# Kernel optimization log

Measured on AMD Instinct MI355X. Metric: run time of the kernel, lower is better.

## Reference

```python
import jax, jax.numpy as jnp
import numpy as np

NUM_NODES = 512
INPUT_DIM = 64
HID_DIM = 64
K_DIFF = 2          # max_diffusion_step
N_LAYERS = 2
N_SUPPORTS = 1      # filter_type='laplacian'
NUM_MATS = N_SUPPORTS * K_DIFF + 1
CONCAT = INPUT_DIM + HID_DIM  # == HID_DIM + HID_DIM since input_dim == hid_dim


def setup_inputs() -> dict:
    key = jax.random.key(0)
    ks = jax.random.split(key, 8)
    T, B = 48, 32
    inputs = jax.random.normal(ks[0], (T, B, NUM_NODES * INPUT_DIM), dtype=jnp.float32)
    h0 = jnp.zeros((N_LAYERS, B, NUM_NODES * HID_DIM), dtype=jnp.float32)
    supports = jax.random.uniform(ks[1], (N_SUPPORTS, NUM_NODES, NUM_NODES), dtype=jnp.float32) / NUM_NODES
    s = 0.05
    W_gate = jax.random.normal(ks[2], (N_LAYERS, NUM_MATS * CONCAT, 2 * HID_DIM), dtype=jnp.float32) * s
    b_gate = jnp.ones((N_LAYERS, 2 * HID_DIM), dtype=jnp.float32)  # bias_start=1.0
    W_c = jax.random.normal(ks[3], (N_LAYERS, NUM_MATS * CONCAT, HID_DIM), dtype=jnp.float32) * s
    b_c = jnp.zeros((N_LAYERS, HID_DIM), dtype=jnp.float32)
    return {"inputs": inputs, "initial_hidden_state": h0, "supports": supports,
            "W_gate": W_gate, "b_gate": b_gate, "W_c": W_c, "b_c": b_c}


def _gconv(supports, x_flat, h_flat, W, b, out_dim):
    # x_flat: (B, N*d_in), h_flat: (B, N*hid)
    B = x_flat.shape[0]
    xh = jnp.concatenate([x_flat.reshape(B, NUM_NODES, -1),
                          h_flat.reshape(B, NUM_NODES, -1)], axis=-1)  # (B,N,c)
    mats = [xh]
    for i in range(N_SUPPORTS):
        S = supports[i]
        t0, t1 = xh, jnp.einsum('nm,bmc->bnc', S, xh)
        mats.append(t1)
        for _ in range(2, K_DIFF + 1):  # Chebyshev recurrence: x_k = 2 S x_{k-1} - x_{k-2}
            t2 = 2.0 * jnp.einsum('nm,bmc->bnc', S, t1) - t0
            mats.append(t2)
            t0, t1 = t1, t2
    feat = jnp.concatenate(mats, axis=-1)            # (B, N, NUM_MATS*c)
    out = jnp.einsum('bnf,fo->bno', feat, W) + b      # (B, N, out_dim)
    return out


def _dcgru_cell(supports, x, h, Wg, bg, Wc, bc):
    B = x.shape[0]
    gates = jax.nn.sigmoid(_gconv(supports, x, h, Wg, bg, 2 * HID_DIM))  # (B,N,2h)
    r, u = jnp.split(gates, 2, axis=-1)
    rh = (r * h.reshape(B, NUM_NODES, HID_DIM)).reshape(B, NUM_NODES * HID_DIM)
    c = jnp.tanh(_gconv(supports, x, rh, Wc, bc, HID_DIM))               # (B,N,h)
    h3 = h.reshape(B, NUM_NODES, HID_DIM)
    new_h = u * h3 + (1.0 - u) * c
    return new_h.reshape(B, NUM_NODES * HID_DIM)


def reference(inputs, initial_hidden_state, supports, W_gate, b_gate, W_c, b_c):
    current = inputs  # (T, B, N*d)
    final_hidden = []
    for l in range(N_LAYERS):
        def step(h, x, l=l):
            h2 = _dcgru_cell(supports, x, h, W_gate[l], b_gate[l], W_c[l], b_c[l])
            return h2, h2
        hT, outs = jax.lax.scan(step, initial_hidden_state[l], current)
        final_hidden.append(hT)
        current = outs
    return jnp.stack(final_hidden, axis=0), current
```

## Files before the change

kernel.cpp:

```cpp
#include <hip/hip_runtime.h>
#include <math.h>

typedef __bf16 bf16_t;
typedef bf16_t bf16x8 __attribute__((ext_vector_type(8)));
typedef bf16_t bf16x4 __attribute__((ext_vector_type(4)));
typedef float  f32x4  __attribute__((ext_vector_type(4)));
typedef unsigned long long u64_t;

#define NB 32
#define NN 512
#define NH 64
#define NF 384
#define TSTEPS 48

static __device__ __forceinline__ f32x4 mfma16(bf16x8 a, bf16x8 b, f32x4 c){
  return __builtin_amdgcn_mfma_f32_16x16x32_bf16(a, b, c, 0, 0, 0);
}
static __device__ __forceinline__ void gload16(char* lds, const char* g){
  __builtin_amdgcn_global_load_lds((const __attribute__((address_space(1))) void*)g,
                                   (__attribute__((address_space(3))) void*)lds, 16, 0, 0);
}
static __device__ __forceinline__ unsigned pack2(float a, float b){
  bf16_t x = (bf16_t)a, y = (bf16_t)b;
  unsigned short ux = __builtin_bit_cast(unsigned short, x);
  unsigned short uy = __builtin_bit_cast(unsigned short, y);
  return (unsigned)ux | ((unsigned)uy << 16);
}

__global__ __launch_bounds__(256) void k_s2f(const float* __restrict__ S,
                                             float* __restrict__ S2f){
  int idx = blockIdx.x * 256 + threadIdx.x;
  int n = idx >> 9, m = idx & 511;
  float acc = 0.f;
  #pragma unroll 8
  for (int k = 0; k < 512; ++k) acc += S[n * 512 + k] * S[k * 512 + m];
  S2f[idx] = acc;
}

__global__ __launch_bounds__(256) void k_prepS(const float* __restrict__ S,
                                               const float* __restrict__ S2f,
                                               char* __restrict__ dst){
  int id = blockIdx.x * 256 + threadIdx.x;
  int r = id >> 9, k = id & 511;
  float v = (r < 512) ? S[r * 512 + k] : S2f[(r - 512) * 512 + k];
  int rt = r >> 5, rr = r & 31, kt = k >> 6, kk = k & 63;
  size_t off = ((size_t)(rt * 8 + kt)) * 4096 + (size_t)(((rr * 128 + 2 * kk)) ^ ((rr & 7) << 4));
  *(bf16_t*)(dst + off) = (bf16_t)v;
}

__global__ __launch_bounds__(256) void k_prepW(const float* __restrict__ W,
                                               char* __restrict__ dst, int OD){
  int i = blockIdx.x * 256 + threadIdx.x;
  int total = 2 * NF * OD;
  if (i >= total) return;
  int l = i / (NF * OD), rem = i - l * (NF * OD);
  int o = rem / NF, f = rem - o * NF;
  const float* Wl = W + (size_t)l * NF * OD;
  float v;
  if (f < 128)      v = Wl[f * OD + o] - Wl[(256 + f) * OD + o];
  else if (f < 256) v = Wl[f * OD + o];
  else              v = 2.f * Wl[f * OD + o];
  int kt = f >> 6, kk = f & 63;
  size_t off = (size_t)l * (6 * OD * 128) + (size_t)kt * (OD * 128)
             + (size_t)(((o * 128 + 2 * kk)) ^ ((o & 7) << 4));
  *(bf16_t*)(dst + off) = (bf16_t)v;
}

__global__ __launch_bounds__(256) void k_hinit(const float* __restrict__ h0,
                                               float* __restrict__ hNf,
                                               bf16_t* __restrict__ hN){
  size_t i = ((size_t)blockIdx.x * 256 + threadIdx.x) * 8;
  f32x4 a = *(const f32x4*)&h0[i], b = *(const f32x4*)&h0[i + 4];
  *(f32x4*)&hNf[i] = a; *(f32x4*)&hNf[i + 4] = b;
  bf16x8 v;
  #pragma unroll
  for (int q = 0; q < 4; ++q){ v[q] = (bf16_t)a[q]; v[q + 4] = (bf16_t)b[q]; }
  *(bf16x8*)&hN[i] = v;
}

__global__ __launch_bounds__(512, 4) void k_gate(
    const float* __restrict__ inputs, const float* __restrict__ curp, int p,
    const bf16_t* __restrict__ hN, const char* __restrict__ SP,
    const char* __restrict__ WgP, const float* __restrict__ bga,
    bf16_t* __restrict__ rhN, float* __restrict__ uN, bf16_t* __restrict__ Dx)
{
  const int l = blockIdx.y;
  const int t = p - l;
  if (t < 0 || t >= TSTEPS) return;

  __shared__ char smem[81920];
  char* const A0 = smem;            char* const A1 = smem + 16384;
  char* const B0 = smem + 32768;    char* const B1 = smem + 49152;
  char* const FT = smem;
  char* const W0 = smem + 49152;    char* const W1 = smem + 65536;
  char* const RL = smem + 49152;
  char* const UL = smem + 57344;

  const int L = blockIdx.x;
  const int b  = (L & 7) + ((L >> 6) << 3);
  const int bx = (L >> 3) & 7;
  const int n0 = bx * 64;
  const int tid = threadIdx.x, lane = tid & 63, w = tid >> 6;
  const int fr = lane & 15, ko = (lane >> 4) * 8, ro = (lane >> 4) * 4;
  const int pp = tid >> 4, q4 = tid & 15;
  const int wr = w >> 2, wc = w & 3;
  const int wn = w & 1, wo = w >> 1;

  const float* xall = l ? curp : inputs;
  const float*  xs = xall + ((size_t)t * NB + b) * NN * NH;
  const bf16_t* hbg = hN + ((size_t)(l * NB + b)) * NN * NH;
  const char* const WgPl = WgP + (size_t)l * 98304;
  const float* const bg = bga + l * 128;
  bf16_t* const rh_l = rhN + (size_t)l * NB * NN * NH;
  float*  const u_l  = uN  + (size_t)l * NB * NN * NH;
  bf16_t* const Dx_l = Dx  + (size_t)l * NB * NN * 128;

  f32x4 acc[4][2] = {};
  f32x4 rx0[2], rx1[2]; u64_t rh0[2], rh1[2];
  char* const Abuf[2] = { A0, A1 };
  char* const Bbuf[2] = { B0, B1 };

  auto ldB = [&](int kt, int s){
    int m = kt * 64 + 2 * pp;
    const float* xr = xs + (size_t)m * NH + q4 * 4;
    rx0[s] = *(const f32x4*)xr; rx1[s] = *(const f32x4*)(xr + NH);
    const bf16_t* hr = hbg + (size_t)m * NH + q4 * 4;
    rh0[s] = *(const u64_t*)hr; rh1[s] = *(const u64_t*)(hr + NH);
  };
  auto stB = [&](int s, char* Bb){
    int mby = 4 * pp;
    #pragma unroll
    for (int i = 0; i < 4; ++i){
      int c = q4 * 4 + i;
      *(unsigned*)(Bb + ((c * 128 + mby) ^ (((c >> 2) & 7) << 4))) = pack2(rx0[s][i], rx1[s][i]);
      int c2 = c + 64;
      unsigned uh = (unsigned)((rh0[s] >> (16 * i)) & 0xffffULL)
                  | ((unsigned)((rh1[s] >> (16 * i)) & 0xffffULL) << 16);
      *(unsigned*)(Bb + ((c2 * 128 + mby) ^ (((c2 >> 2) & 7) << 4))) = uh;
    }
  };
  auto gloadA = [&](int kt, char* Ab){
    #pragma unroll
    for (int i = 0; i < 2; ++i){
      int c = w * 2 + i;
      int ti = c >> 2;
      int rt = (ti < 2) ? (bx * 2 + ti) : (16 + bx * 2 + (ti - 2));
      gload16(Ab + c * 1024,
              SP + ((size_t)(rt * 8 + kt)) * 4096 + (c & 3) * 1024 + lane * 16);
    }
  };
  auto dmm = [&](const char* Ab, const char* Bb){
    #pragma unroll
    for (int kh = 0; kh < 2; ++kh){
      int kb = 2 * (kh * 32 + ko);
      bf16x8 af[4], bf_[2];
      #pragma unroll
      for (int fm = 0; fm < 4; ++fm){
        int r = wr * 64 + fm * 16 + fr;
        af[fm] = *(const bf16x8*)(Ab + (r >> 5) * 4096 + ((((r & 31) * 128 + kb)) ^ ((r & 7) << 4)));
      }
      #pragma unroll
      for (int fc = 0; fc < 2; ++fc){
        int c = wc * 32 + fc * 16 + fr;
        bf_[fc] = *(const bf16x8*)(Bb + ((c * 128 + kb) ^ (((c >> 2) & 7) << 4)));
      }
      #pragma unroll
      for (int fm = 0; fm < 4; ++fm)
        #pragma unroll
        for (int fc = 0; fc < 2; ++fc)
          acc[fm][fc] = mfma16(af[fm], bf_[fc], acc[fm][fc]);
    }
  };

  ldB(0, 0); stB(0, B0);
  ldB(1, 1);
  gloadA(0, A0);
  __syncthreads();

  #pragma unroll
  for (int kt = 0; kt < 8; ++kt){
    if (kt < 7){
      stB((kt + 1) & 1, Bbuf[(kt + 1) & 1]);
      gloadA(kt + 1, Abuf[(kt + 1) & 1]);
    }
    dmm(Abuf[kt & 1], Bbuf[kt & 1]);
    __syncthreads();
    if (kt < 6) ldB(kt + 2, (kt + 2) & 1);
  }

  #pragma unroll
  for (int s = 0; s < 2; ++s){
    int i = tid + s * 512;
    int row = i >> 4, c8 = (i & 15) * 8;
    char* fdst = FT + (((row * 768 + 2 * c8)) ^ ((row & 7) << 4));
    if (c8 < 64){
      const float* xr = xs + (size_t)(n0 + row) * NH + c8;
      f32x4 a = *(const f32x4*)xr, bq = *(const f32x4*)(xr + 4);
      bf16x8 v;
      #pragma unroll
      for (int q = 0; q < 4; ++q){ v[q] = (bf16_t)a[q]; v[q + 4] = (bf16_t)bq[q]; }
      *(bf16x8*)fdst = v;
    } else {
      *(bf16x8*)fdst = *(const bf16x8*)(hbg + (size_t)(n0 + row) * NH + (c8 - 64));
    }
  }
  #pragma unroll
  for (int fm = 0; fm < 4; ++fm)
    #pragma unroll
    for (int fc = 0; fc < 2; ++fc)
      #pragma unroll
      for (int q = 0; q < 4; ++q){
        int dr = wr * 64 + fm * 16 + ro + q;
        int nn = dr & 63;
        int col = ((dr < 64) ? 128 : 256) + wc * 32 + fc * 16 + fr;
        *(bf16_t*)(FT + (((nn * 768 + 2 * col)) ^ ((nn & 7) << 4))) = (bf16_t)acc[fm][fc][q];
      }

  auto gloadW = [&](int j, char* Wb){
    const char* src = WgPl + (size_t)j * 16384 + (w * 64 + lane) * 16;
    gload16(Wb + w * 1024, src);
    gload16(Wb + 8192 + w * 1024, src + 8192);
  };
  gloadW(0, W0);
  __syncthreads();

  #pragma unroll
  for (int s = 0; s < 2; ++s){
    int i = tid + s * 512;
    int row = i >> 4, d8 = (i & 15) * 8;
    int col = (d8 < 64) ? 128 + d8 : 256 + (d8 - 64);
    bf16x8 v = *(const bf16x8*)(FT + (((row * 768 + 2 * col)) ^ ((row & 7) << 4)));
    *(bf16x8*)&Dx_l[((size_t)b * NN + n0 + row) * 128 + d8] = v;
  }

  f32x4 gd[2][2] = {};
  #pragma unroll
  for (int j = 0; j < 6; ++j){
    if (j < 5) gloadW(j + 1, ((j + 1) & 1) ? W1 : W0);
    const char* Wb = (j & 1) ? W1 : W0;
    #pragma unroll
    for (int kh = 0; kh < 2; ++kh){
      int kbf = 2 * (j * 64 + kh * 32 + ko);
      int kbw = 2 * (kh * 32 + ko);
      bf16x8 af[2];
      #pragma unroll
      for (int fm = 0; fm < 2; ++fm){
        int r = wn * 32 + fm * 16 + fr;
        af[fm] = *(const bf16x8*)(FT + ((r * 768 + kbf) ^ ((r & 7) << 4)));
      }
      #pragma unroll
      for (int fo = 0; fo < 2; ++fo){
        int orow = wo * 32 + fo * 16 + fr;
        bf16x8 bw = *(const bf16x8*)(Wb + ((orow * 128 + kbw) ^ ((orow & 7) << 4)));
        #pragma unroll
        for (int fm = 0; fm < 2; ++fm)
          gd[fm][fo] = mfma16(af[fm], bw, gd[fm][fo]);
      }
    }
    __syncthreads();
  }

  #pragma unroll
  for (int fm = 0; fm < 2; ++fm)
    #pragma unroll
    for (int fo = 0; fo < 2; ++fo){
      int o = wo * 32 + fo * 16 + fr;
      float bias = bg[o];
      #pragma unroll
      for (int q = 0; q < 4; ++q){
        int nn = wn * 32 + fm * 16 + ro + q;
        float g = 1.f / (1.f + __expf(-(gd[fm][fo][q] + bias)));
        if (o < 64){
          float hv = (float)*(const bf16_t*)(FT + (((nn * 768 + 2 * (64 + o))) ^ ((nn & 7) << 4)));
          *(bf16_t*)(RL + ((nn * 128 + 2 * o) ^ ((nn & 7) << 4))) = (bf16_t)(g * hv);
        } else {
          *(float*)(UL + ((nn * 256 + 4 * (o - 64)) ^ ((nn & 7) << 5))) = g;
        }
      }
    }
  __syncthreads();
  {
    int row = tid >> 3, o8 = (tid & 7) * 8;
    bf16x8 v = *(const bf16x8*)(RL + ((row * 128 + 2 * o8) ^ ((row & 7) << 4)));
    *(bf16x8*)&rh_l[((size_t)b * NN + n0 + row) * NH + o8] = v;
    int base = (row * 256 + 4 * o8) ^ ((row & 7) << 5);
    f32x4 u0 = *(const f32x4*)(UL + base);
    f32x4 u1 = *(const f32x4*)(UL + base + 16);
    size_t gi = ((size_t)b * NN + n0 + row) * NH + o8;
    *(f32x4*)&u_l[gi] = u0; *(f32x4*)&u_l[gi + 4] = u1;
  }
}

__global__ __launch_bounds__(512, 4) void k_cand(
    const float* __restrict__ inputs, int p,
    const bf16_t* __restrict__ rhN, const bf16_t* __restrict__ Dx,
    const char* __restrict__ SP, const char* __restrict__ WcP,
    const float* __restrict__ bca, const float* __restrict__ uN,
    float* __restrict__ hNf, bf16_t* __restrict__ hN,
    float* __restrict__ outp)
{
  const int l = blockIdx.y;
  const int t = p - l;
  if (t < 0 || t >= TSTEPS) return;

  __shared__ char smem[65536];
  char* const A0 = smem;            char* const A1 = smem + 16384;
  char* const B0 = smem + 32768;    char* const B1 = smem + 40960;
  char* const FT = smem;
  char* const W0 = smem + 49152;    char* const W1 = smem + 57344;
  char* const CL = smem + 49152;

  const int L = blockIdx.x;
  const int b  = (L & 7) + ((L >> 6) << 3);
  const int bx = (L >> 3) & 7;
  const int n0 = bx * 64;
  const int tid = threadIdx.x, lane = tid & 63, w = tid >> 6;
  const int fr = lane & 15, ko = (lane >> 4) * 8, ro = (lane >> 4) * 4;
  const int pp = tid >> 4, q4 = tid & 15;
  const int wr = w >> 2, wc = w & 3;
  const int wn = w & 1, wo = w >> 1;

  float* const cur = outp + (size_t)2 * NB * NN * NH;
  const float* xall = l ? cur : inputs;
  const float*  xs = xall + ((size_t)t * NB + b) * NN * NH;
  const bf16_t* rbg = rhN + ((size_t)(l * NB + b)) * NN * NH;
  const char* const WcPl = WcP + (size_t)l * 49152;
  const float* const bc = bca + l * 64;
  const bf16_t* const Dx_l = Dx + (size_t)l * NB * NN * 128;
  const float* const u_l = uN + (size_t)l * NB * NN * NH;
  float*  const hNf_l = hNf + (size_t)l * NB * NN * NH;
  bf16_t* const hN_l  = hN  + (size_t)l * NB * NN * NH;
  float* const fin = outp + (size_t)l * NB * NN * NH;

  f32x4 ca[4] = {};
  u64_t rh0[2], rh1[2];
  char* const Abuf[2] = { A0, A1 };
  char* const Bbuf[2] = { B0, B1 };

  auto ldB = [&](int kt, int s){
    int m = kt * 64 + 2 * pp;
    const bf16_t* rr = rbg + (size_t)m * NH + q4 * 4;
    rh0[s] = *(const u64_t*)rr; rh1[s] = *(const u64_t*)(rr + NH);
  };
  auto stB = [&](int s, char* Bb){
    int mby = 4 * pp;
    #pragma unroll
    for (int i = 0; i < 4; ++i){
      int c = q4 * 4 + i;
      unsigned u = (unsigned)((rh0[s] >> (16 * i)) & 0xffffULL)
                 | ((unsigned)((rh1[s] >> (16 * i)) & 0xffffULL) << 16);
      *(unsigned*)(Bb + ((c * 128 + mby) ^ (((c >> 2) & 7) << 4))) = u;
    }
  };
  auto gloadA = [&](int kt, char* Ab){
    #pragma unroll
    for (int i = 0; i < 2; ++i){
      int c = w * 2 + i;
      int ti = c >> 2;
      int rt = (ti < 2) ? (bx * 2 + ti) : (16 + bx * 2 + (ti - 2));
      gload16(Ab + c * 1024,
              SP + ((size_t)(rt * 8 + kt)) * 4096 + (c & 3) * 1024 + lane * 16);
    }
  };
  auto cmm = [&](const char* Ab, const char* Bb){
    #pragma unroll
    for (int kh = 0; kh < 2; ++kh){
      int kb = 2 * (kh * 32 + ko);
      int c = wc * 16 + fr;
      bf16x8 bf_ = *(const bf16x8*)(Bb + ((c * 128 + kb) ^ (((c >> 2) & 7) << 4)));
      #pragma unroll
      for (int fm = 0; fm < 4; ++fm){
        int r = wr * 64 + fm * 16 + fr;
        bf16x8 af = *(const bf16x8*)(Ab + (r >> 5) * 4096 + ((((r & 31) * 128 + kb)) ^ ((r & 7) << 4)));
        ca[fm] = mfma16(af, bf_, ca[fm]);
      }
    }
  };

  ldB(0, 0); stB(0, B0);
  ldB(1, 1);
  gloadA(0, A0);
  __syncthreads();

  #pragma unroll
  for (int kt = 0; kt < 8; ++kt){
    if (kt < 7){
      stB((kt + 1) & 1, Bbuf[(kt + 1) & 1]);
      gloadA(kt + 1, Abuf[(kt + 1) & 1]);
    }
    cmm(Abuf[kt & 1], Bbuf[kt & 1]);
    __syncthreads();
    if (kt < 6) ldB(kt + 2, (kt + 2) & 1);
  }

  #pragma unroll
  for (int s = 0; s < 2; ++s){
    int i = tid + s * 512;
    int row = i >> 4, c8 = (i & 15) * 8;
    char* fdst = FT + (((row * 768 + 2 * c8)) ^ ((row & 7) << 4));
    if (c8 < 64){
      const float* xr = xs + (size_t)(n0 + row) * NH + c8;
      f32x4 a = *(const f32x4*)xr, bq = *(const f32x4*)(xr + 4);
      bf16x8 v;
      #pragma unroll
      for (int q = 0; q < 4; ++q){ v[q] = (bf16_t)a[q]; v[q + 4] = (bf16_t)bq[q]; }
      *(bf16x8*)fdst = v;
    } else {
      *(bf16x8*)fdst = *(const bf16x8*)(rbg + (size_t)(n0 + row) * NH + (c8 - 64));
    }
    int col = (c8 < 64) ? 128 + c8 : 256 + (c8 - 64);
    bf16x8 dv = *(const bf16x8*)&Dx_l[((size_t)b * NN + n0 + row) * 128 + c8];
    *(bf16x8*)(FT + (((row * 768 + 2 * col)) ^ ((row & 7) << 4))) = dv;
  }
  #pragma unroll
  for (int fm = 0; fm < 4; ++fm)
    #pragma unroll
    for (int q = 0; q < 4; ++q){
      int dr = wr * 64 + fm * 16 + ro + q;
      int nn = dr & 63;
      int col = ((dr < 64) ? 192 : 320) + wc * 16 + fr;
      *(bf16_t*)(FT + (((nn * 768 + 2 * col)) ^ ((nn & 7) << 4))) = (bf16_t)ca[fm][q];
    }

  auto gloadW = [&](int j, char* Wb){
    gload16(Wb + w * 1024, WcPl + (size_t)j * 8192 + (w * 64 + lane) * 16);
  };
  gloadW(0, W0);
  __syncthreads();

  f32x4 cd[2] = {};
  #pragma unroll
  for (int j = 0; j < 6; ++j){
    if (j < 5) gloadW(j + 1, ((j + 1) & 1) ? W1 : W0);
    const char* Wb = (j & 1) ? W1 : W0;
    #pragma unroll
    for (int kh = 0; kh < 2; ++kh){
      int kbf = 2 * (j * 64 + kh * 32 + ko);
      int kbw = 2 * (kh * 32 + ko);
      int orow = wo * 16 + fr;
      bf16x8 bw = *(const bf16x8*)(Wb + ((orow * 128 + kbw) ^ ((orow & 7) << 4)));
      #pragma unroll
      for (int fm = 0; fm < 2; ++fm){
        int r = wn * 32 + fm * 16 + fr;
        bf16x8 af = *(const bf16x8*)(FT + ((r * 768 + kbf) ^ ((r & 7) << 4)));
        cd[fm] = mfma16(af, bw, cd[fm]);
      }
    }
    __syncthreads();
  }

  #pragma unroll
  for (int fm = 0; fm < 2; ++fm){
    int o = wo * 16 + fr;
    float bias = bc[o];
    #pragma unroll
    for (int q = 0; q < 4; ++q){
      int nn = wn * 32 + fm * 16 + ro + q;
      float e = __expf(2.f * (cd[fm][q] + bias));
      *(float*)(CL + ((nn * 256 + 4 * o) ^ ((nn & 7) << 5))) = (e - 1.f) / (e + 1.f);
    }
  }
  __syncthreads();
  {
    int row = tid >> 3, o8 = (tid & 7) * 8;
    int base = (row * 256 + 4 * o8) ^ ((row & 7) << 5);
    f32x4 c0 = *(const f32x4*)(CL + base);
    f32x4 c1 = *(const f32x4*)(CL + base + 16);
    size_t gi = ((size_t)b * NN + n0 + row) * NH + o8;
    f32x4 u0 = *(const f32x4*)&u_l[gi], u1 = *(const f32x4*)&u_l[gi + 4];
    f32x4 h0v = *(const f32x4*)&hNf_l[gi], h1v = *(const f32x4*)&hNf_l[gi + 4];
    f32x4 n0v, n1v;
    #pragma unroll
    for (int q = 0; q < 4; ++q){
      n0v[q] = u0[q] * h0v[q] + (1.f - u0[q]) * c0[q];
      n1v[q] = u1[q] * h1v[q] + (1.f - u1[q]) * c1[q];
    }
    *(f32x4*)&hNf_l[gi] = n0v; *(f32x4*)&hNf_l[gi + 4] = n1v;
    bf16x8 hb;
    #pragma unroll
    for (int q = 0; q < 4; ++q){ hb[q] = (bf16_t)n0v[q]; hb[q + 4] = (bf16_t)n1v[q]; }
    *(bf16x8*)&hN_l[gi] = hb;
    float* cr = cur + (size_t)t * NB * NN * NH + gi;
    *(f32x4*)cr = n0v; *(f32x4*)(cr + 4) = n1v;
    if (t == TSTEPS - 1){
      *(f32x4*)&fin[gi] = n0v; *(f32x4*)&fin[gi + 4] = n1v;
    }
  }
}

extern "C" void kernel_launch(void* const* d_in, const int* in_sizes, int n_in,
                              void* d_out, int out_size, void* d_ws, size_t ws_size,
                              hipStream_t stream){
  const float* inputs = (const float*)d_in[0];
  const float* h0     = (const float*)d_in[1];
  const float* S      = (const float*)d_in[2];
  const float* W_gate = (const float*)d_in[3];
  const float* b_gate = (const float*)d_in[4];
  const float* W_c    = (const float*)d_in[5];
  const float* b_c    = (const float*)d_in[6];
  float* out = (float*)d_out;
  char* ws = (char*)d_ws;

  char*   SP  =          ws + 0;
  char*   WgP =          ws + 1048576;
  char*   WcP =          ws + 1245184;
  float*  hNf = (float*) (ws + 1343488);
  bf16_t* hN  = (bf16_t*)(ws + 9732096);
  bf16_t* rhN = (bf16_t*)(ws + 13926400);
  float*  uN  = (float*) (ws + 18120704);
  bf16_t* Dx  = (bf16_t*)(ws + 26509312);
  float*  S2f = (float*) (ws + 26509312 + 4194304);

  k_s2f<<<dim3(1024), 256, 0, stream>>>(S, S2f);
  k_prepS<<<dim3(2048), 256, 0, stream>>>(S, S2f, SP);
  k_prepW<<<dim3(384), 256, 0, stream>>>(W_gate, WgP, 128);
  k_prepW<<<dim3(192), 256, 0, stream>>>(W_c, WcP, 64);
  k_hinit<<<dim3(1024), 256, 0, stream>>>(h0, hNf, hN);

  for (int p = 0; p <= TSTEPS; ++p){
    k_gate<<<dim3(256, 2), 512, 0, stream>>>(inputs, out + (size_t)2 * NB * NN * NH,
                                             p, hN, SP, WgP, b_gate, rhN, uN, Dx);
    k_cand<<<dim3(256, 2), 512, 0, stream>>>(inputs, p, rhN, Dx, SP, WcP, b_c, uN,
                                             hNf, hN, out);
  }
}
```

Baseline: 2.217 ms.

## Fuse gate and candidate kernels into skewed per-step kernel across layers

Replaces the separate gate and candidate launches with one k_step kernel per half-step. Each launch runs the gate of one layer alongside the candidate of the other, with layer 1 skewed in time so dependencies still hold. This lets blocks with different resource profiles share the GPU in the same launch and avoid idle tails. It also deepens weight-tile prefetch to two buffers ahead and issues the S-tile async loads before the B staging. All blocks now reserve the larger 80KB shared-memory footprint, and the early weight loads must not overlap LDS regions still in use.

Measured after the change: 2.340 ms. 5.5% more time.

```diff
diff --git a/kernel.cpp b/kernel.cpp
--- a/kernel.cpp
+++ b/kernel.cpp
@@ -78,21 +78,17 @@
   *(bf16x8*)&hN[i] = v;
 }
 
-__global__ __launch_bounds__(512, 4) void k_gate(
-    const float* __restrict__ inputs, const float* __restrict__ curp, int p,
+__device__ __forceinline__ void gate_body(char* smem, int l, int t,
+    const float* __restrict__ inputs, const float* __restrict__ curp,
     const bf16_t* __restrict__ hN, const char* __restrict__ SP,
     const char* __restrict__ WgP, const float* __restrict__ bga,
     bf16_t* __restrict__ rhN, float* __restrict__ uN, bf16_t* __restrict__ Dx)
 {
-  const int l = blockIdx.y;
-  const int t = p - l;
-  if (t < 0 || t >= TSTEPS) return;
-
-  __shared__ char smem[81920];
   char* const A0 = smem;            char* const A1 = smem + 16384;
   char* const B0 = smem + 32768;    char* const B1 = smem + 49152;
   char* const FT = smem;
-  char* const W0 = smem + 49152;    char* const W1 = smem + 65536;
+  char* const W0 = smem + 49152;
+  char* const W1 = smem + 65536;
   char* const RL = smem + 49152;
   char* const UL = smem + 57344;
 
@@ -149,6 +145,11 @@
               SP + ((size_t)(rt * 8 + kt)) * 4096 + (c & 3) * 1024 + lane * 16);
     }
   };
+  auto gloadW = [&](int j, char* Wb){
+    const char* src = WgPl + (size_t)j * 16384 + (w * 64 + lane) * 16;
+    gload16(Wb + w * 1024, src);
+    gload16(Wb + 8192 + w * 1024, src + 8192);
+  };
   auto dmm = [&](const char* Ab, const char* Bb){
     #pragma unroll
     for (int kh = 0; kh < 2; ++kh){
@@ -172,21 +173,23 @@
     }
   };
 
+  gloadA(0, A0);
   ldB(0, 0); stB(0, B0);
   ldB(1, 1);
-  gloadA(0, A0);
   __syncthreads();
 
   #pragma unroll
   for (int kt = 0; kt < 8; ++kt){
     if (kt < 7){
+      gloadA(kt + 1, Abuf[(kt + 1) & 1]);
       stB((kt + 1) & 1, Bbuf[(kt + 1) & 1]);
-      gloadA(kt + 1, Abuf[(kt + 1) & 1]);
     }
     dmm(Abuf[kt & 1], Bbuf[kt & 1]);
     __syncthreads();
     if (kt < 6) ldB(kt + 2, (kt + 2) & 1);
   }
+
+  gloadW(0, W0); gloadW(1, W1);
 
   #pragma unroll
   for (int s = 0; s < 2; ++s){
@@ -215,13 +218,6 @@
         int col = ((dr < 64) ? 128 : 256) + wc * 32 + fc * 16 + fr;
         *(bf16_t*)(FT + (((nn * 768 + 2 * col)) ^ ((nn & 7) << 4))) = (bf16_t)acc[fm][fc][q];
       }
-
-  auto gloadW = [&](int j, char* Wb){
-    const char* src = WgPl + (size_t)j * 16384 + (w * 64 + lane) * 16;
-    gload16(Wb + w * 1024, src);
-    gload16(Wb + 8192 + w * 1024, src + 8192);
-  };
-  gloadW(0, W0);
   __syncthreads();
 
   #pragma unroll
@@ -236,7 +232,6 @@
   f32x4 gd[2][2] = {};
   #pragma unroll
   for (int j = 0; j < 6; ++j){
-    if (j < 5) gloadW(j + 1, ((j + 1) & 1) ? W1 : W0);
     const char* Wb = (j & 1) ? W1 : W0;
     #pragma unroll
     for (int kh = 0; kh < 2; ++kh){
@@ -258,6 +253,7 @@
       }
     }
     __syncthreads();
+    if (j < 4) gloadW(j + 2, (j & 1) ? W1 : W0);
   }
 
   #pragma unroll
@@ -291,19 +287,14 @@
   }
 }
 
-__global__ __launch_bounds__(512, 4) void k_cand(
-    const float* __restrict__ inputs, int p,
+__device__ __forceinline__ void cand_body(char* smem, int l, int t,
+    const float* __restrict__ inputs,
     const bf16_t* __restrict__ rhN, const bf16_t* __restrict__ Dx,
     const char* __restrict__ SP, const char* __restrict__ WcP,
     const float* __restrict__ bca, const float* __restrict__ uN,
     float* __restrict__ hNf, bf16_t* __restrict__ hN,
     float* __restrict__ outp)
 {
-  const int l = blockIdx.y;
-  const int t = p - l;
-  if (t < 0 || t >= TSTEPS) return;
-
-  __shared__ char smem[65536];
   char* const A0 = smem;            char* const A1 = smem + 16384;
   char* const B0 = smem + 32768;    char* const B1 = smem + 40960;
   char* const FT = smem;
@@ -362,6 +353,9 @@
               SP + ((size_t)(rt * 8 + kt)) * 4096 + (c & 3) * 1024 + lane * 16);
     }
   };
+  auto gloadW = [&](int j, char* Wb){
+    gload16(Wb + w * 1024, WcPl + (size_t)j * 8192 + (w * 64 + lane) * 16);
+  };
   auto cmm = [&](const char* Ab, const char* Bb){
     #pragma unroll
     for (int kh = 0; kh < 2; ++kh){
@@ -377,16 +371,17 @@
     }
   };
 
+  gloadA(0, A0);
+  gloadW(0, W0); gloadW(1, W1);
   ldB(0, 0); stB(0, B0);
   ldB(1, 1);
-  gloadA(0, A0);
   __syncthreads();
 
   #pragma unroll
   for (int kt = 0; kt < 8; ++kt){
     if (kt < 7){
+      gloadA(kt + 1, Abuf[(kt + 1) & 1]);
       stB((kt + 1) & 1, Bbuf[(kt + 1) & 1]);
-      gloadA(kt + 1, Abuf[(kt + 1) & 1]);
     }
     cmm(Abuf[kt & 1], Bbuf[kt & 1]);
     __syncthreads();
@@ -421,17 +416,11 @@
       int col = ((dr < 64) ? 192 : 320) + wc * 16 + fr;
       *(bf16_t*)(FT + (((nn * 768 + 2 * col)) ^ ((nn & 7) << 4))) = (bf16_t)ca[fm][q];
     }
-
-  auto gloadW = [&](int j, char* Wb){
-    gload16(Wb + w * 1024, WcPl + (size_t)j * 8192 + (w * 64 + lane) * 16);
-  };
-  gloadW(0, W0);
   __syncthreads();
 
   f32x4 cd[2] = {};
   #pragma unroll
   for (int j = 0; j < 6; ++j){
-    if (j < 5) gloadW(j + 1, ((j + 1) & 1) ? W1 : W0);
     const char* Wb = (j & 1) ? W1 : W0;
     #pragma unroll
     for (int kh = 0; kh < 2; ++kh){
@@ -447,6 +436,7 @@
       }
     }
     __syncthreads();
+    if (j < 4) gloadW(j + 2, (j & 1) ? W1 : W0);
   }
 
   #pragma unroll
@@ -486,6 +476,28 @@
       *(f32x4*)&fin[gi] = n0v; *(f32x4*)&fin[gi + 4] = n1v;
     }
   }
+}
+
+__global__ __launch_bounds__(512, 4) void k_step(int d,
+    const float* __restrict__ inputs, const char* __restrict__ SP,
+    const char* __restrict__ WgP, const char* __restrict__ WcP,
+    const float* __restrict__ bga, const float* __restrict__ bca,
+    bf16_t* __restrict__ rhN, float* __restrict__ uN, bf16_t* __restrict__ Dx,
+    float* __restrict__ hNf, bf16_t* __restrict__ hN, float* __restrict__ outp)
+{
+  __shared__ char smem[81920];
+  const int role = blockIdx.y;
+  const int k = d >> 1;
+  int l, t, g;
+  if (!(d & 1)){
+    if (!role){ g = 1; l = 0; t = k; } else { g = 0; l = 1; t = k - 2; }
+  } else {
+    if (!role){ g = 0; l = 0; t = k; } else { g = 1; l = 1; t = k - 1; }
+  }
+  if (t < 0 || t >= TSTEPS) return;
+  if (g) gate_body(smem, l, t, inputs, outp + (size_t)2 * NB * NN * NH,
+                   hN, SP, WgP, bga, rhN, uN, Dx);
+  else   cand_body(smem, l, t, inputs, rhN, Dx, SP, WcP, bca, uN, hNf, hN, outp);
 }
 
 extern "C" void kernel_launch(void* const* d_in, const int* in_sizes, int n_in,
@@ -517,10 +529,9 @@
   k_prepW<<<dim3(192), 256, 0, stream>>>(W_c, WcP, 64);
   k_hinit<<<dim3(1024), 256, 0, stream>>>(h0, hNf, hN);
 
-  for (int p = 0; p <= TSTEPS; ++p){
-    k_gate<<<dim3(256, 2), 512, 0, stream>>>(inputs, out + (size_t)2 * NB * NN * NH,
-                                             p, hN, SP, WgP, b_gate, rhN, uN, Dx);
-    k_cand<<<dim3(256, 2), 512, 0, stream>>>(inputs, p, rhN, Dx, SP, WcP, b_c, uN,
+  for (int d = 0; d <= 98; ++d){
+    k_step<<<dim3(256, 2), 512, 0, stream>>>(d, inputs, SP, WgP, WcP,
+                                             b_gate, b_c, rhN, uN, Dx,
                                              hNf, hN, out);
   }
 }
```
